# Kernel tuning notes

Measured on AMD Instinct MI355X. Metric: run time of the kernel, lower is better.

## Reference

```python
import jax, jax.numpy as jnp
import numpy as np

D = 128
L_SIZE = 65536
C_SIZE = 32768
E = 262144
N_ITERS = 4


def _mlp(x, w1, b1, w2, b2):
    # 2-layer satbench MLP: Linear -> relu -> Linear
    return jax.nn.relu(x @ w1 + b1) @ w2 + b2


def setup_inputs() -> dict:
    key = jax.random.key(0)
    ks = iter(jax.random.split(key, 32))

    def lin(fi, fo):
        # torch nn.Linear default init, stored as (in, out)
        bound = 1.0 / np.sqrt(fi)
        w = jax.random.uniform(next(ks), (fi, fo), minval=-bound, maxval=bound, dtype=jnp.float32)
        b = jax.random.uniform(next(ks), (fo,), minval=-bound, maxval=bound, dtype=jnp.float32)
        return w, b

    s = np.sqrt(2.0 / D).astype(np.float32)
    inp = {}
    inp['l_edge_index'] = jax.random.randint(next(ks), (E,), 0, L_SIZE, dtype=jnp.int64)
    inp['c_edge_index'] = jax.random.randint(next(ks), (E,), 0, C_SIZE, dtype=jnp.int64)
    inp['l_init'] = jax.random.normal(next(ks), (1, D), dtype=jnp.float32) * s
    inp['c_init'] = jax.random.normal(next(ks), (1, D), dtype=jnp.float32) * s
    inp['w_l2c1'], inp['b_l2c1'] = lin(D, D)
    inp['w_l2c2'], inp['b_l2c2'] = lin(D, D)
    inp['w_c2l1'], inp['b_c2l1'] = lin(D, D)
    inp['w_c2l2'], inp['b_c2l2'] = lin(D, D)
    inp['w_l2l1'], inp['b_l2l1'] = lin(D, D)
    inp['w_l2l2'], inp['b_l2l2'] = lin(D, D)
    inp['w_cu'], inp['b_cu'] = lin(2 * D, D)
    inp['w_lu'], inp['b_lu'] = lin(3 * D, D)
    inp['l_size'] = L_SIZE
    inp['c_size'] = C_SIZE
    return inp


def reference(l_edge_index, c_edge_index, l_init, c_init,
              w_l2c1, b_l2c1, w_l2c2, b_l2c2,
              w_c2l1, b_c2l1, w_c2l2, b_c2l2,
              w_l2l1, b_l2l1, w_l2l2, b_l2l2,
              w_cu, b_cu, w_lu, b_lu, l_size, c_size):
    d = l_init.shape[1]
    ones = jnp.ones((l_edge_index.shape[0], 1), dtype=l_init.dtype)
    l_deg = jax.ops.segment_sum(ones, l_edge_index, num_segments=l_size)   # (L,1)
    c_deg = jax.ops.segment_sum(ones, c_edge_index, num_segments=c_size)   # (C,1)
    degree_norm = jnp.sqrt(l_deg[l_edge_index]) * jnp.sqrt(c_deg[c_edge_index])  # (E,1)

    l_emb = jnp.tile(l_init, (l_size, 1))  # (L,d)
    c_emb = jnp.tile(c_init, (c_size, 1))  # (C,d)

    def step(carry, _):
        l_emb, c_emb = carry
        l2c_msg = _mlp(l_emb, w_l2c1, b_l2c1, w_l2c2, b_l2c2)[l_edge_index]  # (E,d)
        c2l_msg = _mlp(c_emb, w_c2l1, b_c2l1, w_c2l2, b_c2l2)[c_edge_index]  # (E,d)
        # swap positive/negative literal partner embeddings (pairs are adjacent rows)
        l2l_in = l_emb.reshape(l_size // 2, 2, d)[:, ::-1, :].reshape(l_size, d)
        l2l_msg = _mlp(l2l_in, w_l2l1, b_l2l1, w_l2l2, b_l2l2)              # (L,d)
        l2c_aggr = jax.ops.segment_sum(l2c_msg / degree_norm, c_edge_index, num_segments=c_size)
        c_new = jnp.concatenate([c_emb, l2c_aggr], axis=1) @ w_cu + b_cu
        c2l_aggr = jax.ops.segment_sum(c2l_msg / degree_norm, l_edge_index, num_segments=l_size)
        l_new = jnp.concatenate([l_emb, c2l_aggr, l2l_msg], axis=1) @ w_lu + b_lu
        return (l_new, c_new), None

    (l_emb, c_emb), _ = jax.lax.scan(step, (l_emb, c_emb), None, length=N_ITERS)
    return l_emb
```

## Files before the change

### kernel.cpp

```cpp
#include <hip/hip_runtime.h>
#include <hip/hip_bf16.h>

#define D_ 128
#define L_ 65536
#define C_ 32768
#define E_ 262144

typedef __hip_bfloat16 bf16;
typedef __attribute__((ext_vector_type(8))) short short8;
typedef __attribute__((ext_vector_type(4))) float f32x4;

__global__ void detect_k(const unsigned short* __restrict__ wmem,
                         const int* __restrict__ li, int* __restrict__ flags) {
    int t = blockIdx.x * 512 + threadIdx.x;
    if (t < 8192) {
        unsigned short h = wmem[2 * t];
        float v = __bfloat162float(*(const bf16*)&h);
        if (!(fabsf(v) < 0.5f)) atomicOr(&flags[0], 1);
    }
    if (t < 2048) {
        if (li[2 * t + 1] != 0) atomicOr(&flags[1], 1);
    }
}

__device__ __forceinline__ void split2(float v, unsigned short& h, unsigned short& l) {
    bf16 bh = __float2bfloat16(v);
    float fh = __bfloat162float(bh);
    bf16 bl = __float2bfloat16(v - fh);
    h = *(unsigned short*)&bh;
    l = *(unsigned short*)&bl;
}

__device__ __forceinline__ float ldf(const void* s, int i, int isf32) {
    return isf32 ? ((const float*)s)[i] : __bfloat162float(((const bf16*)s)[i]);
}

__global__ void fixdeg_k(const int* __restrict__ ls, const int* __restrict__ cs,
                         int* __restrict__ ld_idx, int* __restrict__ cd_idx,
                         int* __restrict__ ldeg, int* __restrict__ cdeg,
                         const int* __restrict__ flags) {
    int i = blockIdx.x * 256 + threadIdx.x;
    int is32 = flags[1];
    if (i < E_) {
        int v = is32 ? ls[i] : ls[2 * i];
        v = min(max(v, 0), L_ - 1);
        ld_idx[i] = v;
        atomicAdd(&ldeg[v], 1);
    } else {
        int j = i - E_;
        int v = is32 ? cs[j] : cs[2 * j];
        v = min(max(v, 0), C_ - 1);
        cd_idx[j] = v;
        atomicAdd(&cdeg[v], 1);
    }
}

__global__ void cvtwb_k(const void* s0, const void* s1, const void* s2, const void* s3,
                        const void* s4, const void* s5, const void* s6, const void* s7,
                        const void* t0, const void* t1, const void* t2, const void* t3,
                        const void* t4, const void* t5, const void* t6, const void* t7,
                        unsigned short* __restrict__ hi, unsigned short* __restrict__ lo,
                        float* __restrict__ bb, const int* __restrict__ flags) {
    int i = blockIdx.x * 256 + threadIdx.x;
    int isf = flags[0];
    if (i >= 180224) {
        int j = i - 180224;
        const void* src;
        switch (j >> 7) {
            case 0: src = t0; break; case 1: src = t1; break;
            case 2: src = t2; break; case 3: src = t3; break;
            case 4: src = t4; break; case 5: src = t5; break;
            case 6: src = t6; break; default: src = t7; break;
        }
        bb[j] = ldf(src, j & 127, isf);
        return;
    }
    const void* src; int K, base;
    if      (i <  16384) { src = s0; K = 128; base = 0; }
    else if (i <  32768) { src = s1; K = 128; base = 16384; }
    else if (i <  49152) { src = s2; K = 128; base = 32768; }
    else if (i <  65536) { src = s3; K = 128; base = 49152; }
    else if (i <  81920) { src = s4; K = 128; base = 65536; }
    else if (i <  98304) { src = s5; K = 128; base = 81920; }
    else if (i < 131072) { src = s6; K = 256; base = 98304; }
    else                 { src = s7; K = 384; base = 131072; }
    int e = i - base;
    int k = e >> 7, n = e & 127;
    float v = ldf(src, e, isf);
    unsigned short h, l;
    split2(v, h, l);
    hi[base + n * K + k] = h;
    lo[base + n * K + k] = l;
}

__global__ void init2_k(const void* __restrict__ lv, const void* __restrict__ cv,
                        unsigned short* __restrict__ lhi, unsigned short* __restrict__ llo,
                        unsigned short* __restrict__ chi, unsigned short* __restrict__ clo,
                        const int* __restrict__ flags) {
    int i4 = blockIdx.x * 256 + threadIdx.x;
    int isf = flags[0];
    const void* src; unsigned short *dh, *dl; int o;
    if (i4 < L_ * 32) { src = lv; dh = lhi; dl = llo; o = i4; }
    else              { src = cv; dh = chi; dl = clo; o = i4 - L_ * 32; }
    int j = (o & 31) * 4;
    ushort4 vh, vl;
    split2(ldf(src, j + 0, isf), vh.x, vl.x);
    split2(ldf(src, j + 1, isf), vh.y, vl.y);
    split2(ldf(src, j + 2, isf), vh.z, vl.z);
    split2(ldf(src, j + 3, isf), vh.w, vl.w);
    *(ushort4*)&dh[(size_t)o * 4] = vh;
    *(ushort4*)&dl[(size_t)o * 4] = vl;
}

__global__ void scan1b_k(const int* __restrict__ ldeg, const int* __restrict__ cdeg,
                         int* __restrict__ lout, int* __restrict__ cout,
                         int* __restrict__ bsumL, int* __restrict__ bsumC) {
    __shared__ int s[256];
    const int* in; int* out; int* bs; int tile;
    if (blockIdx.x < 256) { in = ldeg; out = lout; bs = bsumL; tile = blockIdx.x; }
    else                  { in = cdeg; out = cout; bs = bsumC; tile = blockIdx.x - 256; }
    int i = tile * 256 + threadIdx.x;
    int v = in[i];
    s[threadIdx.x] = v;
    __syncthreads();
#pragma unroll
    for (int off = 1; off < 256; off <<= 1) {
        int t = (threadIdx.x >= off) ? s[threadIdx.x - off] : 0;
        __syncthreads();
        s[threadIdx.x] += t;
        __syncthreads();
    }
    out[i] = s[threadIdx.x] - v;
    if (threadIdx.x == 255) bs[tile] = s[255];
}

__global__ void scan2b_k(int* __restrict__ bL, int* __restrict__ bC) {
    __shared__ int s[256];
    int* b = blockIdx.x ? bC : bL;
    int nb = blockIdx.x ? 128 : 256;
    int v = (threadIdx.x < nb) ? b[threadIdx.x] : 0;
    s[threadIdx.x] = v;
    __syncthreads();
#pragma unroll
    for (int off = 1; off < 256; off <<= 1) {
        int t = (threadIdx.x >= off) ? s[threadIdx.x - off] : 0;
        __syncthreads();
        s[threadIdx.x] += t;
        __syncthreads();
    }
    if (threadIdx.x < nb) b[threadIdx.x] = s[threadIdx.x] - v;
}

__global__ void scan3b_k(int* __restrict__ lptr, int* __restrict__ cptr,
                         const int* __restrict__ bsumL, const int* __restrict__ bsumC,
                         int* __restrict__ lcur, int* __restrict__ ccur,
                         const int* __restrict__ ldeg, const int* __restrict__ cdeg,
                         float* __restrict__ invsq_l, float* __restrict__ invsq_c) {
    int b = blockIdx.x, t = threadIdx.x;
    if (b < 256) {
        int i = b * 256 + t;
        int v = lptr[i] + bsumL[b];
        lptr[i] = v; lcur[i] = v;
        int d = ldeg[i];
        invsq_l[i] = d ? rsqrtf((float)d) : 0.0f;
    } else {
        int i = (b - 256) * 256 + t;
        int v = cptr[i] + bsumC[b - 256];
        cptr[i] = v; ccur[i] = v;
        int d = cdeg[i];
        invsq_c[i] = d ? rsqrtf((float)d) : 0.0f;
    }
}

__global__ void place_k(const int* __restrict__ li, const int* __restrict__ ci,
                        int* __restrict__ lcur, int* __restrict__ ccur,
                        int* __restrict__ l_other, int* __restrict__ c_other) {
    int e = blockIdx.x * 256 + threadIdx.x;
    if (e >= E_) return;
    int l = li[e], c = ci[e];
    int p = atomicAdd(&ccur[c], 1);
    c_other[p] = l;
    int q = atomicAdd(&lcur[l], 1);
    l_other[q] = c;
}

__global__ __launch_bounds__(256) void gather2_k(
    const int* __restrict__ cptr, const int* __restrict__ cdeg, const int* __restrict__ c_other,
    const unsigned int* __restrict__ lmsg, const float* __restrict__ invsq_c,
    unsigned short* __restrict__ cag_hi, unsigned short* __restrict__ cag_lo,
    const int* __restrict__ lptr, const int* __restrict__ ldeg, const int* __restrict__ l_other,
    const unsigned int* __restrict__ cmsg, const float* __restrict__ invsq_l,
    unsigned short* __restrict__ lag_hi, unsigned short* __restrict__ lag_lo,
    int nC) {
    int node = (blockIdx.x * 256 + threadIdx.x) >> 6;
    int lane = threadIdx.x & 63;
    bool cside = node < nC;
    int j = cside ? node : node - nC;
    const int* ptr = cside ? cptr : lptr;
    const int* dg  = cside ? cdeg : ldeg;
    const int* oth = cside ? c_other : l_other;
    const unsigned int* msg = cside ? lmsg : cmsg;
    float sc = (cside ? invsq_c : invsq_l)[j];
    unsigned short* ohi = cside ? cag_hi : lag_hi;
    unsigned short* olo = cside ? cag_lo : lag_lo;
    int s = ptr[j], cnt = dg[j];
    float2 a0 = {0.f, 0.f}, a1 = {0.f, 0.f};
    int k = 0;
    for (; k + 4 <= cnt; k += 4) {
        int o0 = oth[s + k], o1 = oth[s + k + 1], o2 = oth[s + k + 2], o3 = oth[s + k + 3];
        unsigned int u0 = msg[(size_t)o0 * 64 + lane];
        unsigned int u1 = msg[(size_t)o1 * 64 + lane];
        unsigned int u2 = msg[(size_t)o2 * 64 + lane];
        unsigned int u3 = msg[(size_t)o3 * 64 + lane];
        a0.x += __uint_as_float(u0 << 16) + __uint_as_float(u2 << 16);
        a0.y += __uint_as_float(u0 & 0xffff0000u) + __uint_as_float(u2 & 0xffff0000u);
        a1.x += __uint_as_float(u1 << 16) + __uint_as_float(u3 << 16);
        a1.y += __uint_as_float(u1 & 0xffff0000u) + __uint_as_float(u3 & 0xffff0000u);
    }
    for (; k < cnt; k++) {
        int o = oth[s + k];
        unsigned int u = msg[(size_t)o * 64 + lane];
        a0.x += __uint_as_float(u << 16);
        a0.y += __uint_as_float(u & 0xffff0000u);
    }
    a0.x = (a0.x + a1.x) * sc;
    a0.y = (a0.y + a1.y) * sc;
    unsigned short h0, l0, h1, l1;
    split2(a0.x, h0, l0);
    split2(a0.y, h1, l1);
    ((unsigned int*)ohi)[(size_t)j * 64 + lane] = (unsigned int)h0 | ((unsigned int)h1 << 16);
    ((unsigned int*)olo)[(size_t)j * 64 + lane] = (unsigned int)l0 | ((unsigned int)l1 << 16);
}

__global__ __launch_bounds__(512, 4) void mlp3_k(
    const unsigned short* __restrict__ l_hi, const unsigned short* __restrict__ l_lo,
    const unsigned short* __restrict__ c_hi, const unsigned short* __restrict__ c_lo,
    const unsigned short* __restrict__ wt_hi, const unsigned short* __restrict__ wt_lo,
    const float* __restrict__ bb,
    const float* __restrict__ invsq_l, const float* __restrict__ invsq_c,
    bf16* __restrict__ l_msg, bf16* __restrict__ c_msg, bf16* __restrict__ l2lb,
    int nL, int nC) {
    __shared__ char smem[66048];
    unsigned short (*a_hi)[40] = (unsigned short(*)[40])(smem);
    unsigned short (*a_lo)[40] = (unsigned short(*)[40])(smem + 10240);
    unsigned short* h_hi = (unsigned short*)(smem);
    unsigned short* h_lo = (unsigned short*)(smem + 32768);
    float* scv = (float*)(smem + 65536);

    int b = blockIdx.x, seg, tile;
    if (b < nL)           { seg = 0; tile = b; }
    else if (b < nL + nC) { seg = 1; tile = b - nL; }
    else                  { seg = 2; tile = b - nL - nC; }
    const unsigned short* Ah = (seg == 1) ? c_hi : l_hi;
    const unsigned short* Al = (seg == 1) ? c_lo : l_lo;
    bf16* outp = (seg == 0) ? l_msg : (seg == 1) ? c_msg : l2lb;
    const float* invsq = (seg == 0) ? invsq_l : (seg == 1) ? invsq_c : nullptr;
    const unsigned short* W1h = wt_hi + seg * 32768;
    const unsigned short* W1l = wt_lo + seg * 32768;
    const unsigned short* W2h = W1h + 16384;
    const unsigned short* W2l = W1l + 16384;
    const float* b1v = bb + seg * 256;
    const float* b2v = b1v + 128;
    const int swap = (seg == 2);

    const int t = threadIdx.x;
    const int br0 = tile * 128;
    const int w = t >> 6, lane = t & 63;
    const int wr = w >> 2, wc = w & 3;
    const int quad = lane >> 4, cl = lane & 15;

    if (t < 128) scv[t] = invsq ? invsq[br0 + t] : 1.0f;

    f32x4 acc[4][2];
#pragma unroll
    for (int i = 0; i < 4; i++)
#pragma unroll
        for (int j = 0; j < 2; j++) acc[i][j] = (f32x4){0.f, 0.f, 0.f, 0.f};

    for (int kt = 0; kt < 128; kt += 32) {
#pragma unroll
        for (int i = 0; i < 2; i++) {
            int s = t + 512 * i;
            int r = s >> 3, kq = s & 7;
            int gr = br0 + r;
            if (swap) gr ^= 1;
            *(ushort4*)&a_hi[r][4 * kq] = *(const ushort4*)&Ah[(size_t)gr * D_ + kt + 4 * kq];
            *(ushort4*)&a_lo[r][4 * kq] = *(const ushort4*)&Al[(size_t)gr * D_ + kt + 4 * kq];
        }
        __syncthreads();
        short8 af_h[4], af_l[4];
#pragma unroll
        for (int i = 0; i < 4; i++) {
            int row = 64 * wr + 16 * i + cl;
            af_h[i] = *(const short8*)&a_hi[row][quad * 8];
            af_l[i] = *(const short8*)&a_lo[row][quad * 8];
        }
#pragma unroll
        for (int j = 0; j < 2; j++) {
            int col = 32 * wc + 16 * j + cl;
            short8 bf_h = *(const short8*)&W1h[(size_t)col * 128 + kt + quad * 8];
            short8 bf_l = *(const short8*)&W1l[(size_t)col * 128 + kt + quad * 8];
#pragma unroll
            for (int i = 0; i < 4; i++) {
                acc[i][j] = __builtin_amdgcn_mfma_f32_16x16x32_bf16(af_h[i], bf_h, acc[i][j], 0, 0, 0);
                acc[i][j] = __builtin_amdgcn_mfma_f32_16x16x32_bf16(af_h[i], bf_l, acc[i][j], 0, 0, 0);
                acc[i][j] = __builtin_amdgcn_mfma_f32_16x16x32_bf16(af_l[i], bf_h, acc[i][j], 0, 0, 0);
            }
        }
        __syncthreads();
    }
#pragma unroll
    for (int j = 0; j < 2; j++) {
        int col = 32 * wc + 16 * j + cl;
        float bv = b1v[col];
        int g = col >> 3, go = col & 7;
#pragma unroll
        for (int i = 0; i < 4; i++) {
            int rloc = 64 * wr + 16 * i + quad * 4;
#pragma unroll
            for (int rg = 0; rg < 4; rg++) {
                float v = fmaxf(acc[i][j][rg] + bv, 0.0f);
                unsigned short hh, ll;
                split2(v, hh, ll);
                int r = rloc + rg;
                int off = r * 128 + ((g ^ (r & 15)) << 3) + go;
                h_hi[off] = hh;
                h_lo[off] = ll;
            }
        }
    }
    __syncthreads();
#pragma unroll
    for (int i = 0; i < 4; i++)
#pragma unroll
        for (int j = 0; j < 2; j++) acc[i][j] = (f32x4){0.f, 0.f, 0.f, 0.f};

    for (int kt = 0; kt < 128; kt += 32) {
        short8 af_h[4], af_l[4];
        int gbase = (kt >> 3) + quad;
#pragma unroll
        for (int i = 0; i < 4; i++) {
            int r = 64 * wr + 16 * i + cl;
            int off = r * 128 + ((gbase ^ cl) << 3);
            af_h[i] = *(const short8*)&h_hi[off];
            af_l[i] = *(const short8*)&h_lo[off];
        }
#pragma unroll
        for (int j = 0; j < 2; j++) {
            int col = 32 * wc + 16 * j + cl;
            const short8 bf_h = *(const short8*)&W2h[(size_t)col * 128 + kt + quad * 8];
            const short8 bf_l = *(const short8*)&W2l[(size_t)col * 128 + kt + quad * 8];
#pragma unroll
            for (int i = 0; i < 4; i++) {
                acc[i][j] = __builtin_amdgcn_mfma_f32_16x16x32_bf16(af_h[i], bf_h, acc[i][j], 0, 0, 0);
                acc[i][j] = __builtin_amdgcn_mfma_f32_16x16x32_bf16(af_h[i], bf_l, acc[i][j], 0, 0, 0);
                acc[i][j] = __builtin_amdgcn_mfma_f32_16x16x32_bf16(af_l[i], bf_h, acc[i][j], 0, 0, 0);
            }
        }
    }
#pragma unroll
    for (int j = 0; j < 2; j++) {
        int col = 32 * wc + 16 * j + cl;
        float bv = b2v[col];
#pragma unroll
        for (int i = 0; i < 4; i++) {
            int rloc = 64 * wr + 16 * i + quad * 4;
#pragma unroll
            for (int rg = 0; rg < 4; rg++)
                outp[(size_t)(br0 + rloc + rg) * D_ + col] =
                    __float2bfloat16((acc[i][j][rg] + bv) * scv[rloc + rg]);
        }
    }
}

template <int FINAL>
__global__ __launch_bounds__(256, 2) void update_k(
    const unsigned short* __restrict__ l_hi, const unsigned short* __restrict__ l_lo,
    const unsigned short* __restrict__ c_hi, const unsigned short* __restrict__ c_lo,
    const unsigned short* __restrict__ lag_hi, const unsigned short* __restrict__ lag_lo,
    const unsigned short* __restrict__ cag_hi, const unsigned short* __restrict__ cag_lo,
    const bf16* __restrict__ l2lb,
    const unsigned short* __restrict__ wt_hi, const unsigned short* __restrict__ wt_lo,
    const float* __restrict__ bb,
    unsigned short* __restrict__ c_hi_n, unsigned short* __restrict__ c_lo_n,
    unsigned short* __restrict__ l_hi_n, unsigned short* __restrict__ l_lo_n,
    void* __restrict__ dout, const int* __restrict__ flags) {
    __shared__ unsigned short a_hi[2][128][40], a_lo[2][128][40];
    const int t = threadIdx.x;
    int b = blockIdx.x;
    const bool cseg = (!FINAL) && (b < 256);
    const int tile = (FINAL || cseg) ? b : b - 256;
    const int K = cseg ? 256 : 384;
    const int NK = K >> 5;
    const unsigned short* A0h = cseg ? c_hi : l_hi;
    const unsigned short* A0l = cseg ? c_lo : l_lo;
    const unsigned short* AGh = cseg ? cag_hi : lag_hi;
    const unsigned short* AGl = cseg ? cag_lo : lag_lo;
    const unsigned short* Wh = wt_hi + (cseg ? 98304 : 131072);
    const unsigned short* Wl = wt_lo + (cseg ? 98304 : 131072);
    const float* bias = bb + (cseg ? 768 : 896);
    const int br0 = tile * 128;
    const int w = t >> 6, lane = t & 63;
    const int wr = w >> 1, wc = w & 1;
    const int quad = lane >> 4, cl = lane & 15;
    const int sr = t >> 3, skq = t & 7;

    f32x4 acc[4][4];
#pragma unroll
    for (int i = 0; i < 4; i++)
#pragma unroll
        for (int j = 0; j < 4; j++) acc[i][j] = (f32x4){0.f, 0.f, 0.f, 0.f};

#pragma unroll
    for (int i = 0; i < 4; i++) {
        size_t go = (size_t)(br0 + sr + 32 * i) * D_ + 4 * skq;
        *(ushort4*)&a_hi[0][sr + 32 * i][4 * skq] = *(const ushort4*)&A0h[go];
        *(ushort4*)&a_lo[0][sr + 32 * i][4 * skq] = *(const ushort4*)&A0l[go];
    }
    __syncthreads();

    for (int kt = 0; kt < NK; kt++) {
        const int p = kt & 1;
        const bool haslo = (kt < 8);
        const bool hasnext = (kt + 1 < NK);
        const bool nlo = (kt + 1 < 8);
        ushort4 nh[4], nl[4];
        if (hasnext) {
            const int kn = kt + 1;
            const unsigned short* sh;
            const unsigned short* sl = nullptr;
            int koff;
            if (kn < 4)      { sh = A0h; sl = A0l; koff = kn * 32; }
            else if (kn < 8) { sh = AGh; sl = AGl; koff = (kn - 4) * 32; }
            else             { sh = (const unsigned short*)l2lb; koff = (kn - 8) * 32; }
#pragma unroll
            for (int i = 0; i < 4; i++) {
                size_t go = (size_t)(br0 + sr + 32 * i) * D_ + koff + 4 * skq;
                nh[i] = *(const ushort4*)&sh[go];
                if (nlo) nl[i] = *(const ushort4*)&sl[go];
            }
        }
        short8 af_h[4], af_l[4];
#pragma unroll
        for (int i = 0; i < 4; i++) {
            int row = 64 * wr + 16 * i + cl;
            af_h[i] = *(const short8*)&a_hi[p][row][quad * 8];
            if (haslo) af_l[i] = *(const short8*)&a_lo[p][row][quad * 8];
        }
#pragma unroll
        for (int j = 0; j < 4; j++) {
            int col = 64 * wc + 16 * j + cl;
            const short8 bf_h = *(const short8*)&Wh[(size_t)col * K + kt * 32 + quad * 8];
            const short8 bf_l = *(const short8*)&Wl[(size_t)col * K + kt * 32 + quad * 8];
#pragma unroll
            for (int i = 0; i < 4; i++) {
                acc[i][j] = __builtin_amdgcn_mfma_f32_16x16x32_bf16(af_h[i], bf_h, acc[i][j], 0, 0, 0);
                acc[i][j] = __builtin_amdgcn_mfma_f32_16x16x32_bf16(af_h[i], bf_l, acc[i][j], 0, 0, 0);
                if (haslo)
                    acc[i][j] = __builtin_amdgcn_mfma_f32_16x16x32_bf16(af_l[i], bf_h, acc[i][j], 0, 0, 0);
            }
        }
        if (hasnext) {
#pragma unroll
            for (int i = 0; i < 4; i++) {
                *(ushort4*)&a_hi[p ^ 1][sr + 32 * i][4 * skq] = nh[i];
                if (nlo) *(ushort4*)&a_lo[p ^ 1][sr + 32 * i][4 * skq] = nl[i];
            }
        }
        __syncthreads();
    }
    const int f32out = FINAL ? flags[0] : 1;
    unsigned short* Oh = cseg ? c_hi_n : l_hi_n;
    unsigned short* Ol = cseg ? c_lo_n : l_lo_n;
#pragma unroll
    for (int j = 0; j < 4; j++) {
        int col = 64 * wc + 16 * j + cl;
        float bv = bias[col];
#pragma unroll
        for (int i = 0; i < 4; i++) {
            int rbase = br0 + 64 * wr + 16 * i + quad * 4;
#pragma unroll
            for (int rg = 0; rg < 4; rg++) {
                float v = acc[i][j][rg] + bv;
                size_t idx = (size_t)(rbase + rg) * D_ + col;
                if (FINAL) {
                    if (f32out) ((float*)dout)[idx] = v;
                    else        ((bf16*)dout)[idx] = __float2bfloat16(v);
                } else {
                    unsigned short hh, ll;
                    split2(v, hh, ll);
                    Oh[idx] = hh;
                    Ol[idx] = ll;
                }
            }
        }
    }
}

extern "C" void kernel_launch(void* const* d_in, const int* in_sizes, int n_in,
                              void* d_out, int out_size, void* d_ws, size_t ws_size,
                              hipStream_t stream) {
    const int* li_raw = (const int*)d_in[0];
    const int* ci_raw = (const int*)d_in[1];

    const size_t LD = (size_t)L_ * D_;
    const size_t CD = (size_t)C_ * D_;
    unsigned short* us = (unsigned short*)d_ws;
    unsigned short* l_hi[2] = { us,          us + 2 * LD };
    unsigned short* l_lo[2] = { us + LD,     us + 3 * LD };
    unsigned short* c_hi[2] = { us + 4 * LD,          us + 4 * LD + 2 * CD };
    unsigned short* c_lo[2] = { us + 4 * LD + CD,     us + 4 * LD + 3 * CD };
    unsigned short* lag_hi = us + 4 * LD + 4 * CD;
    unsigned short* lag_lo = lag_hi + LD;
    unsigned short* cag_hi = lag_lo + LD;
    unsigned short* cag_lo = cag_hi + CD;
    bf16* l2lb_p = (bf16*)(cag_lo + CD);
    float* invsq_l = (float*)((unsigned short*)l2lb_p + LD);
    float* invsq_c = invsq_l + L_;
    float* bb    = invsq_c + C_;
    unsigned short* wt_hi = (unsigned short*)(bb + 1024);
    unsigned short* wt_lo = wt_hi + 180224;
    int*   li    = (int*)(wt_lo + 180224);
    int*   ci    = li + E_;
    int*   l_other = ci + E_;
    int*   c_other = l_other + E_;
    int*   ldegi = c_other + E_;
    int*   cdegi = ldegi + L_;
    int*   lptr  = cdegi + C_;
    int*   cptr  = lptr + L_;
    int*   lcur  = cptr + C_;
    int*   ccur  = lcur + L_;
    int*   bsumL = ccur + C_;
    int*   bsumC = bsumL + 256;
    int*   flags = bsumC + 128;

    hipMemsetAsync(flags, 0, 2 * sizeof(int), stream);
    detect_k<<<16, 512, 0, stream>>>((const unsigned short*)d_in[4], li_raw, flags);

    hipMemsetAsync(ldegi, 0, (size_t)(L_ + C_) * sizeof(int), stream);
    fixdeg_k<<<2 * E_ / 256, 256, 0, stream>>>(li_raw, ci_raw, li, ci, ldegi, cdegi, flags);

    cvtwb_k<<<708, 256, 0, stream>>>(d_in[4], d_in[6], d_in[8], d_in[10], d_in[12],
                                     d_in[14], d_in[16], d_in[18],
                                     d_in[5], d_in[7], d_in[9], d_in[11], d_in[13],
                                     d_in[15], d_in[17], d_in[19], wt_hi, wt_lo, bb, flags);

    scan1b_k<<<384, 256, 0, stream>>>(ldegi, cdegi, lptr, cptr, bsumL, bsumC);
    scan2b_k<<<2, 256, 0, stream>>>(bsumL, bsumC);
    scan3b_k<<<384, 256, 0, stream>>>(lptr, cptr, bsumL, bsumC, lcur, ccur,
                                      ldegi, cdegi, invsq_l, invsq_c);
    place_k<<<E_ / 256, 256, 0, stream>>>(li, ci, lcur, ccur, l_other, c_other);

    init2_k<<<(L_ + C_) * 32 / 256, 256, 0, stream>>>(
        d_in[2], d_in[3], l_hi[0], l_lo[0], c_hi[0], c_lo[0], flags);

    const int nL = L_ / 128, nC = C_ / 128;
    int cur = 0;
    for (int it = 0; it < 3; it++) {
        int nxt = cur ^ 1;
        mlp3_k<<<2 * nL + nC, 512, 0, stream>>>(
            l_hi[cur], l_lo[cur], c_hi[cur], c_lo[cur], wt_hi, wt_lo, bb,
            invsq_l, invsq_c,
            (bf16*)l_lo[nxt], (bf16*)c_lo[nxt], l2lb_p, nL, nC);
        gather2_k<<<(C_ + L_) / 4, 256, 0, stream>>>(
            cptr, cdegi, c_other, (const unsigned int*)l_lo[nxt], invsq_c, cag_hi, cag_lo,
            lptr, ldegi, l_other, (const unsigned int*)c_lo[nxt], invsq_l, lag_hi, lag_lo, C_);
        update_k<0><<<768, 256, 0, stream>>>(
            l_hi[cur], l_lo[cur], c_hi[cur], c_lo[cur],
            lag_hi, lag_lo, cag_hi, cag_lo, l2lb_p, wt_hi, wt_lo, bb,
            c_hi[nxt], c_lo[nxt], l_hi[nxt], l_lo[nxt], nullptr, flags);
        cur = nxt;
    }
    int nxt = cur ^ 1;
    mlp3_k<<<nC + nL, 512, 0, stream>>>(
        l_hi[cur], l_lo[cur], c_hi[cur], c_lo[cur], wt_hi, wt_lo, bb,
        invsq_l, invsq_c,
        (bf16*)l_lo[nxt], (bf16*)c_lo[nxt], l2lb_p, 0, nC);
    gather2_k<<<L_ / 4, 256, 0, stream>>>(
        cptr, cdegi, c_other, (const unsigned int*)l_lo[nxt], invsq_c, cag_hi, cag_lo,
        lptr, ldegi, l_other, (const unsigned int*)c_lo[nxt], invsq_l, lag_hi, lag_lo, 0);
    update_k<1><<<512, 256, 0, stream>>>(
        l_hi[cur], l_lo[cur], c_hi[cur], c_lo[cur],
        lag_hi, lag_lo, cag_hi, cag_lo, l2lb_p, wt_hi, wt_lo, bb,
        nullptr, nullptr, nullptr, nullptr, d_out, flags);
}
```

Before: 732.5 us.

## Stage GEMM A-tiles via direct global-to-LDS loads with XOR swizzle

Both the MLP and update kernels now load activation tiles with global_load_lds (16-byte direct-to-LDS) into an XOR-swizzled layout instead of register-staged copies into padded arrays. The MLP kernel loads the whole 128x128 hi/lo tile once up front, which removes the per-k-step syncs. The update kernel keeps its double buffer but issues async LDS fills, shrinks its LDS, and raises launch_bounds to allow 4 blocks per SM. This cuts register pressure and VGPR round-trips. The risk is correctness of the async-load waits, since only __syncthreads guards the LDS fill.

Result: no change. 722.0 us (-1.4%).

```diff
diff --git a/kernel.cpp b/kernel.cpp
--- a/kernel.cpp
+++ b/kernel.cpp
@@ -9,6 +9,14 @@
 typedef __hip_bfloat16 bf16;
 typedef __attribute__((ext_vector_type(8))) short short8;
 typedef __attribute__((ext_vector_type(4))) float f32x4;
+
+__device__ __forceinline__ void gl2lds16(const void* g, void* l) {
+    __builtin_amdgcn_global_load_lds(
+        (const __attribute__((address_space(1))) unsigned int*)g,
+        (__attribute__((address_space(3))) unsigned int*)l, 16, 0, 0);
+}
+
+__device__ __forceinline__ int uswz(int r) { return (r + (r >> 2)) & 3; }
 
 __global__ void detect_k(const unsigned short* __restrict__ wmem,
                          const int* __restrict__ li, int* __restrict__ flags) {
@@ -241,8 +249,6 @@
     bf16* __restrict__ l_msg, bf16* __restrict__ c_msg, bf16* __restrict__ l2lb,
     int nL, int nC) {
     __shared__ char smem[66048];
-    unsigned short (*a_hi)[40] = (unsigned short(*)[40])(smem);
-    unsigned short (*a_lo)[40] = (unsigned short(*)[40])(smem + 10240);
     unsigned short* h_hi = (unsigned short*)(smem);
     unsigned short* h_lo = (unsigned short*)(smem + 32768);
     float* scv = (float*)(smem + 65536);
@@ -269,37 +275,44 @@
     const int wr = w >> 2, wc = w & 3;
     const int quad = lane >> 4, cl = lane & 15;
 
-    if (t < 128) scv[t] = invsq ? invsq[br0 + t] : 1.0f;
-
-    f32x4 acc[4][2];
-#pragma unroll
-    for (int i = 0; i < 4; i++)
-#pragma unroll
-        for (int j = 0; j < 2; j++) acc[i][j] = (f32x4){0.f, 0.f, 0.f, 0.f};
-
-    for (int kt = 0; kt < 128; kt += 32) {
-#pragma unroll
-        for (int i = 0; i < 2; i++) {
-            int s = t + 512 * i;
-            int r = s >> 3, kq = s & 7;
+    {
+        const unsigned short* P = (w & 1) ? Al : Ah;
+        const int s = w >> 1;
+        char* sb = smem + s * 16384 + (w & 1) * 8192;
+#pragma unroll
+        for (int c = 0; c < 8; c++) {
+            int r = c * 16 + (lane >> 2);
+            int g = (lane & 3) ^ uswz(r);
             int gr = br0 + r;
             if (swap) gr ^= 1;
-            *(ushort4*)&a_hi[r][4 * kq] = *(const ushort4*)&Ah[(size_t)gr * D_ + kt + 4 * kq];
-            *(ushort4*)&a_lo[r][4 * kq] = *(const ushort4*)&Al[(size_t)gr * D_ + kt + 4 * kq];
-        }
-        __syncthreads();
+            gl2lds16(&P[(size_t)gr * D_ + s * 32 + g * 8], sb + c * 1024);
+        }
+    }
+    if (t < 128) scv[t] = invsq ? invsq[br0 + t] : 1.0f;
+
+    f32x4 acc[4][2];
+#pragma unroll
+    for (int i = 0; i < 4; i++)
+#pragma unroll
+        for (int j = 0; j < 2; j++) acc[i][j] = (f32x4){0.f, 0.f, 0.f, 0.f};
+
+    __syncthreads();
+
+    for (int kt = 0; kt < 4; kt++) {
+        const char* bh = smem + kt * 16384;
         short8 af_h[4], af_l[4];
 #pragma unroll
         for (int i = 0; i < 4; i++) {
             int row = 64 * wr + 16 * i + cl;
-            af_h[i] = *(const short8*)&a_hi[row][quad * 8];
-            af_l[i] = *(const short8*)&a_lo[row][quad * 8];
+            int so = row * 64 + ((quad ^ uswz(row)) << 4);
+            af_h[i] = *(const short8*)(bh + so);
+            af_l[i] = *(const short8*)(bh + 8192 + so);
         }
 #pragma unroll
         for (int j = 0; j < 2; j++) {
             int col = 32 * wc + 16 * j + cl;
-            short8 bf_h = *(const short8*)&W1h[(size_t)col * 128 + kt + quad * 8];
-            short8 bf_l = *(const short8*)&W1l[(size_t)col * 128 + kt + quad * 8];
+            short8 bf_h = *(const short8*)&W1h[(size_t)col * 128 + kt * 32 + quad * 8];
+            short8 bf_l = *(const short8*)&W1l[(size_t)col * 128 + kt * 32 + quad * 8];
 #pragma unroll
             for (int i = 0; i < 4; i++) {
                 acc[i][j] = __builtin_amdgcn_mfma_f32_16x16x32_bf16(af_h[i], bf_h, acc[i][j], 0, 0, 0);
@@ -307,8 +320,8 @@
                 acc[i][j] = __builtin_amdgcn_mfma_f32_16x16x32_bf16(af_l[i], bf_h, acc[i][j], 0, 0, 0);
             }
         }
-        __syncthreads();
-    }
+    }
+    __syncthreads();
 #pragma unroll
     for (int j = 0; j < 2; j++) {
         int col = 32 * wc + 16 * j + cl;
@@ -374,7 +387,7 @@
 }
 
 template <int FINAL>
-__global__ __launch_bounds__(256, 2) void update_k(
+__global__ __launch_bounds__(256, 4) void update_k(
     const unsigned short* __restrict__ l_hi, const unsigned short* __restrict__ l_lo,
     const unsigned short* __restrict__ c_hi, const unsigned short* __restrict__ c_lo,
     const unsigned short* __restrict__ lag_hi, const unsigned short* __restrict__ lag_lo,
@@ -385,7 +398,7 @@
     unsigned short* __restrict__ c_hi_n, unsigned short* __restrict__ c_lo_n,
     unsigned short* __restrict__ l_hi_n, unsigned short* __restrict__ l_lo_n,
     void* __restrict__ dout, const int* __restrict__ flags) {
-    __shared__ unsigned short a_hi[2][128][40], a_lo[2][128][40];
+    __shared__ char smem[32768];
     const int t = threadIdx.x;
     int b = blockIdx.x;
     const bool cseg = (!FINAL) && (b < 256);
@@ -403,7 +416,23 @@
     const int w = t >> 6, lane = t & 63;
     const int wr = w >> 1, wc = w & 1;
     const int quad = lane >> 4, cl = lane & 15;
-    const int sr = t >> 3, skq = t & 7;
+
+    auto stage = [&](int kn, int pb) {
+        const unsigned short* sh; const unsigned short* sl = nullptr; int koff;
+        bool lo = true;
+        if (kn < 4)      { sh = A0h; sl = A0l; koff = kn * 32; }
+        else if (kn < 8) { sh = AGh; sl = AGl; koff = (kn - 4) * 32; }
+        else             { sh = (const unsigned short*)l2lb; koff = (kn - 8) * 32; lo = false; }
+        char* hb = smem + pb * 16384;
+#pragma unroll
+        for (int c = 0; c < 2; c++) {
+            int r = w * 32 + c * 16 + (lane >> 2);
+            int g = (lane & 3) ^ uswz(r);
+            size_t go = (size_t)(br0 + r) * D_ + koff + g * 8;
+            gl2lds16(&sh[go], hb + w * 2048 + c * 1024);
+            if (lo) gl2lds16(&sl[go], hb + 8192 + w * 2048 + c * 1024);
+        }
+    };
 
     f32x4 acc[4][4];
 #pragma unroll
@@ -411,41 +440,21 @@
 #pragma unroll
         for (int j = 0; j < 4; j++) acc[i][j] = (f32x4){0.f, 0.f, 0.f, 0.f};
 
-#pragma unroll
-    for (int i = 0; i < 4; i++) {
-        size_t go = (size_t)(br0 + sr + 32 * i) * D_ + 4 * skq;
-        *(ushort4*)&a_hi[0][sr + 32 * i][4 * skq] = *(const ushort4*)&A0h[go];
-        *(ushort4*)&a_lo[0][sr + 32 * i][4 * skq] = *(const ushort4*)&A0l[go];
-    }
+    stage(0, 0);
     __syncthreads();
 
     for (int kt = 0; kt < NK; kt++) {
         const int p = kt & 1;
         const bool haslo = (kt < 8);
-        const bool hasnext = (kt + 1 < NK);
-        const bool nlo = (kt + 1 < 8);
-        ushort4 nh[4], nl[4];
-        if (hasnext) {
-            const int kn = kt + 1;
-            const unsigned short* sh;
-            const unsigned short* sl = nullptr;
-            int koff;
-            if (kn < 4)      { sh = A0h; sl = A0l; koff = kn * 32; }
-            else if (kn < 8) { sh = AGh; sl = AGl; koff = (kn - 4) * 32; }
-            else             { sh = (const unsigned short*)l2lb; koff = (kn - 8) * 32; }
-#pragma unroll
-            for (int i = 0; i < 4; i++) {
-                size_t go = (size_t)(br0 + sr + 32 * i) * D_ + koff + 4 * skq;
-                nh[i] = *(const ushort4*)&sh[go];
-                if (nlo) nl[i] = *(const ushort4*)&sl[go];
-            }
-        }
+        if (kt + 1 < NK) stage(kt + 1, p ^ 1);
+        const char* hb = smem + p * 16384;
         short8 af_h[4], af_l[4];
 #pragma unroll
         for (int i = 0; i < 4; i++) {
             int row = 64 * wr + 16 * i + cl;
-            af_h[i] = *(const short8*)&a_hi[p][row][quad * 8];
-            if (haslo) af_l[i] = *(const short8*)&a_lo[p][row][quad * 8];
+            int so = row * 64 + ((quad ^ uswz(row)) << 4);
+            af_h[i] = *(const short8*)(hb + so);
+            if (haslo) af_l[i] = *(const short8*)(hb + 8192 + so);
         }
 #pragma unroll
         for (int j = 0; j < 4; j++) {
@@ -458,13 +467,6 @@
                 acc[i][j] = __builtin_amdgcn_mfma_f32_16x16x32_bf16(af_h[i], bf_l, acc[i][j], 0, 0, 0);
                 if (haslo)
                     acc[i][j] = __builtin_amdgcn_mfma_f32_16x16x32_bf16(af_l[i], bf_h, acc[i][j], 0, 0, 0);
-            }
-        }
-        if (hasnext) {
-#pragma unroll
-            for (int i = 0; i < 4; i++) {
-                *(ushort4*)&a_hi[p ^ 1][sr + 32 * i][4 * skq] = nh[i];
-                if (nlo) *(ushort4*)&a_lo[p ^ 1][sr + 32 * i][4 * skq] = nl[i];
             }
         }
         __syncthreads();
```
